# Performance work log

Measured on AMD Instinct MI355X. Metric: run time of the kernel, lower is better.

## Reference

```python
import jax, jax.numpy as jnp
import numpy as np

B, T, DIM, H, DH = 4, 4096, 1024, 16, 64


def setup_inputs() -> dict:
    key = jax.random.key(0)
    ks = jax.random.split(key, 6)
    s = lambda fan_in: 1.0 / np.sqrt(fan_in)
    x = jax.random.normal(ks[0], (B, T, DIM), dtype=jnp.float32)
    Wq = jax.random.uniform(ks[1], (DIM, H * DH), jnp.float32, -s(DIM), s(DIM))
    Wk = jax.random.uniform(ks[2], (DIM, H * DH), jnp.float32, -s(DIM), s(DIM))
    Wv = jax.random.uniform(ks[3], (DIM, H * DH), jnp.float32, -s(DIM), s(DIM))
    Wo = jax.random.uniform(ks[4], (H * DH, DIM), jnp.float32, -s(H * DH), s(H * DH))
    bo = jax.random.uniform(ks[5], (DIM,), jnp.float32, -s(H * DH), s(H * DH))
    return {"x": x, "Wq": Wq, "Wk": Wk, "Wv": Wv, "Wo": Wo, "bo": bo}


def reference(x, Wq, Wk, Wv, Wo, bo):
    b, t, _ = x.shape
    # projections (no bias, matching nn.Linear(bias=False))
    to_heads = lambda y: y.reshape(b, t, H, DH).transpose(0, 2, 1, 3)  # bhnd
    q = to_heads(x @ Wq)
    k = to_heads(x @ Wk)
    v = to_heads(x @ Wv)
    # linear attention: softmax over feature dim for q, over seq dim for k
    q = jax.nn.softmax(q, axis=-1) * (DH ** -0.5)
    k = jax.nn.softmax(k, axis=-2)
    context = jnp.einsum('bhnd,bhne->bhde', k, v)   # [b,h,dh,dh]
    attn = jnp.einsum('bhnd,bhde->bhne', q, context)  # [b,h,n,dh]
    attn = attn.transpose(0, 2, 1, 3).reshape(b, t, H * DH)
    return attn @ Wo + bo  # dropout is identity at p=0.0 / eval
```

## Files before the change

kernel.cpp:

```cpp
#include <hip/hip_runtime.h>
#include <hip/hip_bf16.h>
#include <cstdint>
#include <cstddef>

#define BB 4
#define TT 4096
#define HH 16
#define NROWS 16384

typedef __attribute__((ext_vector_type(8))) short bf16x8;
typedef __attribute__((ext_vector_type(4))) float f32x4;

__device__ __forceinline__ void gload_lds16(const void* g, void* l) {
  __builtin_amdgcn_global_load_lds(
      (const __attribute__((address_space(1))) void*)g,
      (__attribute__((address_space(3))) void*)l, 16, 0, 0);
}

template <int N>
__device__ __forceinline__ void wait_vmcnt() {
  if constexpr (N == 4)
    asm volatile("s_waitcnt vmcnt(4)" ::: "memory");
  else
    asm volatile("s_waitcnt vmcnt(0)" ::: "memory");
  __builtin_amdgcn_sched_barrier(0);
}

__device__ __forceinline__ void hbar() {
  asm volatile("s_barrier" ::: "memory");
  __builtin_amdgcn_sched_barrier(0);
}

__global__ __launch_bounds__(256) void xconv_k(const float* __restrict__ x,
                                               __hip_bfloat16* __restrict__ xb) {
  const size_t i = ((size_t)blockIdx.x * 256 + threadIdx.x) * 8;
  float4 a = *(const float4*)&x[i];
  float4 b = *(const float4*)&x[i + 4];
  __hip_bfloat16 o[8] __attribute__((aligned(16)));
  o[0] = __float2bfloat16(a.x); o[1] = __float2bfloat16(a.y);
  o[2] = __float2bfloat16(a.z); o[3] = __float2bfloat16(a.w);
  o[4] = __float2bfloat16(b.x); o[5] = __float2bfloat16(b.y);
  o[6] = __float2bfloat16(b.z); o[7] = __float2bfloat16(b.w);
  *(int4*)&xb[i] = *(const int4*)o;
}

__global__ __launch_bounds__(256) void wconv_k(const float* __restrict__ Wq,
                                               const float* __restrict__ Wk,
                                               const float* __restrict__ Wv,
                                               const float* __restrict__ Wo,
                                               __hip_bfloat16* __restrict__ WT) {
  const int which = blockIdx.z;
  const float* W = which == 0 ? Wq : which == 1 ? Wk : which == 2 ? Wv : Wo;
  __shared__ float tile[64][65];
  const int n0 = blockIdx.x * 64, k0 = blockIdx.y * 64;
  const int t = threadIdx.x;
  const int r = t >> 2;
  const int cq = (t & 3) * 16;
#pragma unroll
  for (int i = 0; i < 4; ++i) {
    float4 v = *(const float4*)&W[(size_t)(k0 + r) * 1024 + n0 + cq + i * 4];
    tile[r][cq + i * 4 + 0] = v.x;
    tile[r][cq + i * 4 + 1] = v.y;
    tile[r][cq + i * 4 + 2] = v.z;
    tile[r][cq + i * 4 + 3] = v.w;
  }
  __syncthreads();
  __hip_bfloat16 ob[16] __attribute__((aligned(16)));
#pragma unroll
  for (int j = 0; j < 16; ++j) ob[j] = __float2bfloat16(tile[cq + j][r]);
  __hip_bfloat16* dst = WT + (size_t)(which * 1024 + n0 + r) * 1024 + k0 + cq;
  *(int4*)dst = *(const int4*)&ob[0];
  *(int4*)(dst + 8) = *(const int4*)&ob[8];
}

template <int OMODE, int PB>
__global__ __launch_bounds__(512) void mgemm3_k(
    const __hip_bfloat16* __restrict__ A, int lda,
    const __hip_bfloat16* __restrict__ BT, const float* __restrict__ bias,
    void* __restrict__ Cp, int ldc, int gx) {
  __shared__ __hip_bfloat16 lds[2][32768];

  const int t = threadIdx.x;
  const int wid = t >> 6, l = t & 63;
  const int wr = wid >> 2, wc = wid & 3;

  const int nwg = gridDim.x;
  const int cpx = nwg >> 3;
  const int bid = blockIdx.x;
  const int swz = (bid & 7) * cpx + (bid >> 3);
  const int bx = swz % gx, by = swz / gx;
  const int row0 = by * 256, col0 = bx * 256;

  const __hip_bfloat16* BTb = PB ? BT + ((size_t)(row0 >> 12) << 20) : BT;

  const int sg = l >> 3;
  const int octp = ((l & 7) + sg) & 7;
  const int koct = octp & 3;
  const int srow = 2 * (wid * 16 + sg) + (octp >> 2);
  const __hip_bfloat16* As0 = A + (size_t)(row0 + srow) * lda + koct * 8;
  const __hip_bfloat16* Bs0 = BTb + (size_t)(col0 + srow) * 1024 + koct * 8;

  f32x4 acc[8][4];
#pragma unroll
  for (int m = 0; m < 8; ++m)
#pragma unroll
    for (int n = 0; n < 4; ++n) acc[m][n] = (f32x4){0.f, 0.f, 0.f, 0.f};

  const int lr = l & 15, hk = l >> 4;
  const int slot = (((lr & 1) << 2) + hk - (lr >> 1)) & 7;
  const int rdo = (lr >> 1) * 64 + slot * 8;

  auto stageA = [&](int tn, int c) {
    __hip_bfloat16* d = &lds[tn & 1][c * 8192 + wid * 1024];
    const __hip_bfloat16* s = As0 + tn * 64 + c * 32;
    gload_lds16(s, d);
    gload_lds16(s + (size_t)16 * lda, d + 512);
  };
  auto stageB = [&](int tn, int c) {
    __hip_bfloat16* d = &lds[tn & 1][16384 + c * 8192 + wid * 1024];
    const __hip_bfloat16* s = Bs0 + tn * 64 + c * 32;
    gload_lds16(s, d);
    gload_lds16(s + (size_t)16 * 1024, d + 512);
  };

  stageA(0, 0); stageB(0, 0); stageA(0, 1); stageB(0, 1);

  const __hip_bfloat16* sb = &lds[0][0];
  for (int tn = 0; tn < 16; ++tn) {
    const int bufo = (tn & 1) * 32768;
    const bool pre = tn < 15;
    bf16x8 bfv[4], afv[4];

    wait_vmcnt<4>();
    hbar();
    if (pre) stageA(tn + 1, 0);
#pragma unroll
    for (int n = 0; n < 4; ++n)
      bfv[n] = *(const bf16x8*)(sb + bufo + 16384 + wc * 2048 + n * 512 + rdo);
#pragma unroll
    for (int j = 0; j < 4; ++j)
      afv[j] = *(const bf16x8*)(sb + bufo + wr * 4096 + j * 512 + rdo);
    __builtin_amdgcn_s_setprio(1);
#pragma unroll
    for (int j = 0; j < 4; ++j)
#pragma unroll
      for (int n = 0; n < 4; ++n)
        acc[j][n] = __builtin_amdgcn_mfma_f32_16x16x32_bf16(afv[j], bfv[n],
                                                            acc[j][n], 0, 0, 0);
    __builtin_amdgcn_s_setprio(0);
    if (pre) stageB(tn + 1, 0);
#pragma unroll
    for (int j = 0; j < 4; ++j)
      afv[j] = *(const bf16x8*)(sb + bufo + wr * 4096 + 2048 + j * 512 + rdo);
    __builtin_amdgcn_s_setprio(1);
#pragma unroll
    for (int j = 0; j < 4; ++j)
#pragma unroll
      for (int n = 0; n < 4; ++n)
        acc[4 + j][n] = __builtin_amdgcn_mfma_f32_16x16x32_bf16(
            afv[j], bfv[n], acc[4 + j][n], 0, 0, 0);
    __builtin_amdgcn_s_setprio(0);

    if (pre)
      wait_vmcnt<4>();
    else
      wait_vmcnt<0>();
    hbar();
    if (pre) stageA(tn + 1, 1);
#pragma unroll
    for (int n = 0; n < 4; ++n)
      bfv[n] = *(const bf16x8*)(sb + bufo + 8192 + 16384 + wc * 2048 +
                                n * 512 + rdo);
#pragma unroll
    for (int j = 0; j < 4; ++j)
      afv[j] = *(const bf16x8*)(sb + bufo + 8192 + wr * 4096 + j * 512 + rdo);
    __builtin_amdgcn_s_setprio(1);
#pragma unroll
    for (int j = 0; j < 4; ++j)
#pragma unroll
      for (int n = 0; n < 4; ++n)
        acc[j][n] = __builtin_amdgcn_mfma_f32_16x16x32_bf16(afv[j], bfv[n],
                                                            acc[j][n], 0, 0, 0);
    __builtin_amdgcn_s_setprio(0);
    if (pre) stageB(tn + 1, 1);
#pragma unroll
    for (int j = 0; j < 4; ++j)
      afv[j] = *(const bf16x8*)(sb + bufo + 8192 + wr * 4096 + 2048 + j * 512 +
                                rdo);
    __builtin_amdgcn_s_setprio(1);
#pragma unroll
    for (int j = 0; j < 4; ++j)
#pragma unroll
      for (int n = 0; n < 4; ++n)
        acc[4 + j][n] = __builtin_amdgcn_mfma_f32_16x16x32_bf16(
            afv[j], bfv[n], acc[4 + j][n], 0, 0, 0);
    __builtin_amdgcn_s_setprio(0);
  }

  const int cr = hk * 4;
  const int cc = lr;
  if constexpr (OMODE == 0) {
    __hip_bfloat16* C = (__hip_bfloat16*)Cp;
#pragma unroll
    for (int m = 0; m < 8; ++m)
#pragma unroll
      for (int n = 0; n < 4; ++n) {
        const size_t cb = (size_t)(row0 + wr * 128 + m * 16 + cr) * ldc +
                          col0 + wc * 64 + n * 16 + cc;
#pragma unroll
        for (int j = 0; j < 4; ++j)
          C[cb + (size_t)j * ldc] = __float2bfloat16(acc[m][n][j]);
      }
  } else {
    float* C = (float*)Cp;
    float bv[4];
#pragma unroll
    for (int n = 0; n < 4; ++n) bv[n] = bias[col0 + wc * 64 + n * 16 + cc];
#pragma unroll
    for (int m = 0; m < 8; ++m)
#pragma unroll
      for (int n = 0; n < 4; ++n) {
        const size_t cb = (size_t)(row0 + wr * 128 + m * 16 + cr) * ldc +
                          col0 + wc * 64 + n * 16 + cc;
#pragma unroll
        for (int j = 0; j < 4; ++j)
          C[cb + (size_t)j * ldc] = acc[m][n][j] + bv[n];
      }
  }
}

__global__ __launch_bounds__(256) void ctxq_k(__hip_bfloat16* __restrict__ qkv,
                                              float* __restrict__ part,
                                              float* __restrict__ den) {
  __shared__ __hip_bfloat16 ldsb[2 * 8736];
  __hip_bfloat16* ekT = ldsb;
  __hip_bfloat16* vfT = ldsb + 8736;

  const int bh = blockIdx.x;
  const int s = blockIdx.y;
  const int b = bh >> 4;
  const int h = bh & 15;
  const int n0 = s * 128;
  const int t = threadIdx.x;

  const int rr = t >> 1;
  const int c0 = (t & 1) * 32;
  const size_t base = (size_t)(b * TT + n0 + rr) * 3072 + 1024 + h * 64 + c0;
  int4 kq[4], vq[4];
#pragma unroll
  for (int i = 0; i < 4; ++i) {
    kq[i] = *(const int4*)(qkv + base + i * 8);
    vq[i] = *(const int4*)(qkv + base + 1024 + i * 8);
  }

  {
    const int g8 = t >> 3;
    const int lc = (t & 7) * 8;
#pragma unroll
    for (int it = 0; it < 4; ++it) {
      const int r = it * 32 + g8;
      __hip_bfloat16* p =
          qkv + (size_t)(b * TT + n0 + r) * 3072 + h * 64 + lc;
      int4 raw = *(const int4*)p;
      const __hip_bfloat16* bp = (const __hip_bfloat16*)&raw;
      float v[8];
      float m = -1e30f;
#pragma unroll
      for (int j = 0; j < 8; ++j) {
        v[j] = __bfloat162float(bp[j]);
        m = fmaxf(m, v[j]);
      }
      m = fmaxf(m, __shfl_xor(m, 1));
      m = fmaxf(m, __shfl_xor(m, 2));
      m = fmaxf(m, __shfl_xor(m, 4));
      float sm = 0.f;
#pragma unroll
      for (int j = 0; j < 8; ++j) {
        v[j] = __expf(v[j] - m);
        sm += v[j];
      }
      sm += __shfl_xor(sm, 1);
      sm += __shfl_xor(sm, 2);
      sm += __shfl_xor(sm, 4);
      const float inv = 0.125f / sm;
      __hip_bfloat16 o[8] __attribute__((aligned(16)));
#pragma unroll
      for (int j = 0; j < 8; ++j) o[j] = __float2bfloat16(v[j] * inv);
      *(int4*)p = *(const int4*)o;
    }
  }

#pragma unroll
  for (int i = 0; i < 4; ++i) {
    const __hip_bfloat16* kp = (const __hip_bfloat16*)&kq[i];
    const __hip_bfloat16* vp = (const __hip_bfloat16*)&vq[i];
#pragma unroll
    for (int j = 0; j < 8; ++j) {
      const int c = c0 + i * 8 + j;
      const int off = c * 136 + ((c >> 5) & 1) * 32 + rr;
      ekT[off] = __float2bfloat16(__expf(__bfloat162float(kp[j])));
      vfT[off] = vp[j];
    }
  }
  __syncthreads();

  const int w = t >> 6, l = t & 63;
  const int lr = l & 15, hk = l >> 4;
  f32x4 acc[4];
#pragma unroll
  for (int n = 0; n < 4; ++n) acc[n] = (f32x4){0.f, 0.f, 0.f, 0.f};

  const int arow = w * 16 + lr;
  const int abase = arow * 136 + ((arow >> 5) & 1) * 32 + hk * 8;
#pragma unroll
  for (int ks = 0; ks < 4; ++ks) {
    bf16x8 af = *(const bf16x8*)(ekT + abase + ks * 32);
#pragma unroll
    for (int n = 0; n < 4; ++n) {
      const int brow = n * 16 + lr;
      bf16x8 bf = *(const bf16x8*)(vfT + brow * 136 + ((brow >> 5) & 1) * 32 +
                                   hk * 8 + ks * 32);
      acc[n] =
          __builtin_amdgcn_mfma_f32_16x16x32_bf16(af, bf, acc[n], 0, 0, 0);
    }
  }

  float* pb = part + ((size_t)bh * 32 + s) * 4096;
#pragma unroll
  for (int n = 0; n < 4; ++n)
#pragma unroll
    for (int j = 0; j < 4; ++j)
      pb[(w * 16 + hk * 4 + j) * 64 + n * 16 + lr] = acc[n][j];

  if ((t & 3) == 0) {
    const int d = t >> 2;
    const int dbase = d * 136 + ((d >> 5) & 1) * 32;
    float sden = 0.f;
#pragma unroll
    for (int q8 = 0; q8 < 16; ++q8) {
      bf16x8 e8 = *(const bf16x8*)(ekT + dbase + q8 * 8);
      const __hip_bfloat16* ep = (const __hip_bfloat16*)&e8;
#pragma unroll
      for (int j = 0; j < 8; ++j) sden += __bfloat162float(ep[j]);
    }
    den[((size_t)bh * 32 + s) * 64 + d] = sden;
  }
}

__global__ __launch_bounds__(256) void ctx_reduce_k(
    const float* __restrict__ part, const float* __restrict__ den,
    __hip_bfloat16* __restrict__ ctxb) {
  const int bh = blockIdx.x, q = blockIdx.y, t = threadIdx.x;
  const int idx = q * 1024 + t * 4;
  const int d = idx >> 6;
  float sden = 0.f;
  for (int s = 0; s < 32; ++s) sden += den[((size_t)bh * 32 + s) * 64 + d];
  float4 sv = {0.f, 0.f, 0.f, 0.f};
  const float* pb = part + (size_t)bh * 32 * 4096 + idx;
  for (int s = 0; s < 32; ++s) {
    float4 v = *(const float4*)(pb + (size_t)s * 4096);
    sv.x += v.x; sv.y += v.y; sv.z += v.z; sv.w += v.w;
  }
  const float di = 1.0f / sden;
  __hip_bfloat16 ob[4] __attribute__((aligned(8)));
  ob[0] = __float2bfloat16(sv.x * di);
  ob[1] = __float2bfloat16(sv.y * di);
  ob[2] = __float2bfloat16(sv.z * di);
  ob[3] = __float2bfloat16(sv.w * di);
  *(int2*)&ctxb[(size_t)bh * 4096 + idx] = *(const int2*)ob;
}

__global__ __launch_bounds__(256) void wfuse_k(
    const __hip_bfloat16* __restrict__ WT,
    const __hip_bfloat16* __restrict__ ctxb, __hip_bfloat16* __restrict__ WfT) {
  const int bh = blockIdx.x;
  const int b = bh >> 4, h = bh & 15;
  const int t = threadIdx.x, w = t >> 6, l = t & 63;
  const int n1 = blockIdx.y * 64 + w * 16;
  const int lr = l & 15, hk = l >> 4;

  f32x4 acc[4];
#pragma unroll
  for (int n = 0; n < 4; ++n) acc[n] = (f32x4){0.f, 0.f, 0.f, 0.f};

  const __hip_bfloat16* Abase =
      WT + (size_t)(3072 + n1 + lr) * 1024 + h * 64 + hk * 8;
  const __hip_bfloat16* Bbase = ctxb + (size_t)bh * 4096 + hk * 8;

#pragma unroll
  for (int kk2 = 0; kk2 < 2; ++kk2) {
    bf16x8 af = *(const bf16x8*)(Abase + kk2 * 32);
#pragma unroll
    for (int n = 0; n < 4; ++n) {
      bf16x8 bf = *(const bf16x8*)(Bbase + (n * 16 + lr) * 64 + kk2 * 32);
      acc[n] = __builtin_amdgcn_mfma_f32_16x16x32_bf16(af, bf, acc[n], 0, 0, 0);
    }
  }

  __hip_bfloat16* W0 = WfT + ((size_t)b << 20) + (size_t)(n1 + hk * 4) * 1024 +
                       h * 64 + lr;
#pragma unroll
  for (int n = 0; n < 4; ++n)
#pragma unroll
    for (int j = 0; j < 4; ++j)
      W0[(size_t)j * 1024 + n * 16] = __float2bfloat16(acc[n][j]);
}

extern "C" void kernel_launch(void* const* d_in, const int* in_sizes, int n_in,
                              void* d_out, int out_size, void* d_ws,
                              size_t ws_size, hipStream_t stream) {
  const float* x = (const float*)d_in[0];
  const float* Wq = (const float*)d_in[1];
  const float* Wk = (const float*)d_in[2];
  const float* Wv = (const float*)d_in[3];
  const float* Wo = (const float*)d_in[4];
  const float* bo = (const float*)d_in[5];
  float* out = (float*)d_out;

  char* ws = (char*)d_ws;
  __hip_bfloat16* qkv = (__hip_bfloat16*)ws;
  __hip_bfloat16* WT = (__hip_bfloat16*)(ws + 100663296ull);
  float* den = (float*)(ws + 100663296ull + 8388608ull);
  __hip_bfloat16* ctxb =
      (__hip_bfloat16*)(ws + 100663296ull + 8388608ull + 524288ull);
  __hip_bfloat16* WfT =
      (__hip_bfloat16*)(ws + 100663296ull + 8388608ull + 1048576ull);
  __hip_bfloat16* xb = (__hip_bfloat16*)d_out;
  float* part = (float*)((char*)d_out + 33554432ull);

  const dim3 blk(256);

  xconv_k<<<dim3(NROWS * 1024 / 8 / 256), blk, 0, stream>>>(x, xb);
  wconv_k<<<dim3(16, 16, 4), blk, 0, stream>>>(Wq, Wk, Wv, Wo, WT);

  mgemm3_k<0, 0><<<dim3(768), dim3(512), 0, stream>>>(xb, 1024, WT, nullptr,
                                                      qkv, 3072, 12);

  ctxq_k<<<dim3(64, 32), blk, 0, stream>>>(qkv, part, den);
  ctx_reduce_k<<<dim3(64, 4), blk, 0, stream>>>(part, den, ctxb);
  wfuse_k<<<dim3(64, 16), blk, 0, stream>>>(WT, ctxb, WfT);

  mgemm3_k<1, 1><<<dim3(256), dim3(512), 0, stream>>>(qkv, 3072, WfT, bo, out,
                                                      1024, 4);
}
```

Baseline: 195.4 us.

## Use 4-stage LDS pipeline in GEMM and fuse Q softmax into QKV epilogue

The GEMM drops its 2-buffer, 64-wide K-step scheme for a 4-slot ring of 32-wide K-steps, keeping three stages of global-to-LDS loads in flight and needing one barrier per step. The QKV GEMM epilogue now applies the per-head feature softmax and scaling to Q in registers, using cross-lane shuffles, before storing. This removes the separate read-modify-write pass over Q in the context kernel, which now only reads qkv. The costs are more barriers per unit of K, extra exp and shuffle work in the Q-column tiles, and Q being rounded to bf16 after the softmax instead of before it.

Result: slower. 203.3 us (+4.0%).

```diff
diff --git a/kernel.cpp b/kernel.cpp
--- a/kernel.cpp
+++ b/kernel.cpp
@@ -19,7 +19,9 @@
 
 template <int N>
 __device__ __forceinline__ void wait_vmcnt() {
-  if constexpr (N == 4)
+  if constexpr (N == 8)
+    asm volatile("s_waitcnt vmcnt(8)" ::: "memory");
+  else if constexpr (N == 4)
     asm volatile("s_waitcnt vmcnt(4)" ::: "memory");
   else
     asm volatile("s_waitcnt vmcnt(0)" ::: "memory");
@@ -73,12 +75,12 @@
   *(int4*)(dst + 8) = *(const int4*)&ob[8];
 }
 
-template <int OMODE, int PB>
-__global__ __launch_bounds__(512) void mgemm3_k(
+template <int OMODE, int PB, int QSM>
+__global__ __launch_bounds__(512) void mgemm4_k(
     const __hip_bfloat16* __restrict__ A, int lda,
     const __hip_bfloat16* __restrict__ BT, const float* __restrict__ bias,
     void* __restrict__ Cp, int ldc, int gx) {
-  __shared__ __hip_bfloat16 lds[2][32768];
+  __shared__ __hip_bfloat16 lds[4][16384];
 
   const int t = threadIdx.x;
   const int wid = t >> 6, l = t & 63;
@@ -110,36 +112,25 @@
   const int slot = (((lr & 1) << 2) + hk - (lr >> 1)) & 7;
   const int rdo = (lr >> 1) * 64 + slot * 8;
 
-  auto stageA = [&](int tn, int c) {
-    __hip_bfloat16* d = &lds[tn & 1][c * 8192 + wid * 1024];
-    const __hip_bfloat16* s = As0 + tn * 64 + c * 32;
-    gload_lds16(s, d);
-    gload_lds16(s + (size_t)16 * lda, d + 512);
+  auto stage = [&](int u) {
+    __hip_bfloat16* d = &lds[u & 3][wid * 1024];
+    const __hip_bfloat16* sa = As0 + u * 32;
+    const __hip_bfloat16* sb = Bs0 + u * 32;
+    gload_lds16(sa, d);
+    gload_lds16(sa + (size_t)16 * lda, d + 512);
+    gload_lds16(sb, d + 8192);
+    gload_lds16(sb + (size_t)16 * 1024, d + 8192 + 512);
   };
-  auto stageB = [&](int tn, int c) {
-    __hip_bfloat16* d = &lds[tn & 1][16384 + c * 8192 + wid * 1024];
-    const __hip_bfloat16* s = Bs0 + tn * 64 + c * 32;
-    gload_lds16(s, d);
-    gload_lds16(s + (size_t)16 * 1024, d + 512);
-  };
-
-  stageA(0, 0); stageB(0, 0); stageA(0, 1); stageB(0, 1);
-
-  const __hip_bfloat16* sb = &lds[0][0];
-  for (int tn = 0; tn < 16; ++tn) {
-    const int bufo = (tn & 1) * 32768;
-    const bool pre = tn < 15;
+
+  auto compute = [&](int sl) {
+    const __hip_bfloat16* s = &lds[sl][0];
     bf16x8 bfv[4], afv[4];
-
-    wait_vmcnt<4>();
-    hbar();
-    if (pre) stageA(tn + 1, 0);
 #pragma unroll
     for (int n = 0; n < 4; ++n)
-      bfv[n] = *(const bf16x8*)(sb + bufo + 16384 + wc * 2048 + n * 512 + rdo);
-#pragma unroll
-    for (int j = 0; j < 4; ++j)
-      afv[j] = *(const bf16x8*)(sb + bufo + wr * 4096 + j * 512 + rdo);
+      bfv[n] = *(const bf16x8*)(s + 8192 + wc * 2048 + n * 512 + rdo);
+#pragma unroll
+    for (int j = 0; j < 4; ++j)
+      afv[j] = *(const bf16x8*)(s + wr * 4096 + j * 512 + rdo);
     __builtin_amdgcn_s_setprio(1);
 #pragma unroll
     for (int j = 0; j < 4; ++j)
@@ -148,10 +139,9 @@
         acc[j][n] = __builtin_amdgcn_mfma_f32_16x16x32_bf16(afv[j], bfv[n],
                                                             acc[j][n], 0, 0, 0);
     __builtin_amdgcn_s_setprio(0);
-    if (pre) stageB(tn + 1, 0);
-#pragma unroll
-    for (int j = 0; j < 4; ++j)
-      afv[j] = *(const bf16x8*)(sb + bufo + wr * 4096 + 2048 + j * 512 + rdo);
+#pragma unroll
+    for (int j = 0; j < 4; ++j)
+      afv[j] = *(const bf16x8*)(s + wr * 4096 + 2048 + j * 512 + rdo);
     __builtin_amdgcn_s_setprio(1);
 #pragma unroll
     for (int j = 0; j < 4; ++j)
@@ -160,46 +150,53 @@
         acc[4 + j][n] = __builtin_amdgcn_mfma_f32_16x16x32_bf16(
             afv[j], bfv[n], acc[4 + j][n], 0, 0, 0);
     __builtin_amdgcn_s_setprio(0);
-
-    if (pre)
-      wait_vmcnt<4>();
-    else
-      wait_vmcnt<0>();
+  };
+
+  stage(0); stage(1); stage(2);
+
+#pragma unroll 4
+  for (int u = 0; u < 28; ++u) {
+    wait_vmcnt<8>();
     hbar();
-    if (pre) stageA(tn + 1, 1);
-#pragma unroll
-    for (int n = 0; n < 4; ++n)
-      bfv[n] = *(const bf16x8*)(sb + bufo + 8192 + 16384 + wc * 2048 +
-                                n * 512 + rdo);
-#pragma unroll
-    for (int j = 0; j < 4; ++j)
-      afv[j] = *(const bf16x8*)(sb + bufo + 8192 + wr * 4096 + j * 512 + rdo);
-    __builtin_amdgcn_s_setprio(1);
-#pragma unroll
-    for (int j = 0; j < 4; ++j)
-#pragma unroll
-      for (int n = 0; n < 4; ++n)
-        acc[j][n] = __builtin_amdgcn_mfma_f32_16x16x32_bf16(afv[j], bfv[n],
-                                                            acc[j][n], 0, 0, 0);
-    __builtin_amdgcn_s_setprio(0);
-    if (pre) stageB(tn + 1, 1);
-#pragma unroll
-    for (int j = 0; j < 4; ++j)
-      afv[j] = *(const bf16x8*)(sb + bufo + 8192 + wr * 4096 + 2048 + j * 512 +
-                                rdo);
-    __builtin_amdgcn_s_setprio(1);
-#pragma unroll
-    for (int j = 0; j < 4; ++j)
-#pragma unroll
-      for (int n = 0; n < 4; ++n)
-        acc[4 + j][n] = __builtin_amdgcn_mfma_f32_16x16x32_bf16(
-            afv[j], bfv[n], acc[4 + j][n], 0, 0, 0);
-    __builtin_amdgcn_s_setprio(0);
-  }
+    stage(u + 3);
+    compute(u & 3);
+  }
+  wait_vmcnt<8>(); hbar(); stage(31); compute(0);
+  wait_vmcnt<8>(); hbar(); compute(1);
+  wait_vmcnt<4>(); hbar(); compute(2);
+  wait_vmcnt<0>(); hbar(); compute(3);
 
   const int cr = hk * 4;
   const int cc = lr;
   if constexpr (OMODE == 0) {
+    if (QSM && col0 < 1024) {
+#pragma unroll
+      for (int m = 0; m < 8; ++m) {
+#pragma unroll
+        for (int j = 0; j < 4; ++j) {
+          float mx = fmaxf(fmaxf(acc[m][0][j], acc[m][1][j]),
+                           fmaxf(acc[m][2][j], acc[m][3][j]));
+          mx = fmaxf(mx, __shfl_xor(mx, 1));
+          mx = fmaxf(mx, __shfl_xor(mx, 2));
+          mx = fmaxf(mx, __shfl_xor(mx, 4));
+          mx = fmaxf(mx, __shfl_xor(mx, 8));
+          float e0 = __expf(acc[m][0][j] - mx);
+          float e1 = __expf(acc[m][1][j] - mx);
+          float e2 = __expf(acc[m][2][j] - mx);
+          float e3 = __expf(acc[m][3][j] - mx);
+          float sm = e0 + e1 + e2 + e3;
+          sm += __shfl_xor(sm, 1);
+          sm += __shfl_xor(sm, 2);
+          sm += __shfl_xor(sm, 4);
+          sm += __shfl_xor(sm, 8);
+          const float inv = 0.125f / sm;
+          acc[m][0][j] = e0 * inv;
+          acc[m][1][j] = e1 * inv;
+          acc[m][2][j] = e2 * inv;
+          acc[m][3][j] = e3 * inv;
+        }
+      }
+    }
     __hip_bfloat16* C = (__hip_bfloat16*)Cp;
 #pragma unroll
     for (int m = 0; m < 8; ++m)
@@ -229,9 +226,9 @@
   }
 }
 
-__global__ __launch_bounds__(256) void ctxq_k(__hip_bfloat16* __restrict__ qkv,
-                                              float* __restrict__ part,
-                                              float* __restrict__ den) {
+__global__ __launch_bounds__(256) void ctxkv_k(
+    const __hip_bfloat16* __restrict__ qkv, float* __restrict__ part,
+    float* __restrict__ den) {
   __shared__ __hip_bfloat16 ldsb[2 * 8736];
   __hip_bfloat16* ekT = ldsb;
   __hip_bfloat16* vfT = ldsb + 8736;
@@ -251,43 +248,6 @@
   for (int i = 0; i < 4; ++i) {
     kq[i] = *(const int4*)(qkv + base + i * 8);
     vq[i] = *(const int4*)(qkv + base + 1024 + i * 8);
-  }
-
-  {
-    const int g8 = t >> 3;
-    const int lc = (t & 7) * 8;
-#pragma unroll
-    for (int it = 0; it < 4; ++it) {
-      const int r = it * 32 + g8;
-      __hip_bfloat16* p =
-          qkv + (size_t)(b * TT + n0 + r) * 3072 + h * 64 + lc;
-      int4 raw = *(const int4*)p;
-      const __hip_bfloat16* bp = (const __hip_bfloat16*)&raw;
-      float v[8];
-      float m = -1e30f;
-#pragma unroll
-      for (int j = 0; j < 8; ++j) {
-        v[j] = __bfloat162float(bp[j]);
-        m = fmaxf(m, v[j]);
-      }
-      m = fmaxf(m, __shfl_xor(m, 1));
-      m = fmaxf(m, __shfl_xor(m, 2));
-      m = fmaxf(m, __shfl_xor(m, 4));
-      float sm = 0.f;
-#pragma unroll
-      for (int j = 0; j < 8; ++j) {
-        v[j] = __expf(v[j] - m);
-        sm += v[j];
-      }
-      sm += __shfl_xor(sm, 1);
-      sm += __shfl_xor(sm, 2);
-      sm += __shfl_xor(sm, 4);
-      const float inv = 0.125f / sm;
-      __hip_bfloat16 o[8] __attribute__((aligned(16)));
-#pragma unroll
-      for (int j = 0; j < 8; ++j) o[j] = __float2bfloat16(v[j] * inv);
-      *(int4*)p = *(const int4*)o;
-    }
   }
 
 #pragma unroll
@@ -433,13 +393,13 @@
   xconv_k<<<dim3(NROWS * 1024 / 8 / 256), blk, 0, stream>>>(x, xb);
   wconv_k<<<dim3(16, 16, 4), blk, 0, stream>>>(Wq, Wk, Wv, Wo, WT);
 
-  mgemm3_k<0, 0><<<dim3(768), dim3(512), 0, stream>>>(xb, 1024, WT, nullptr,
-                                                      qkv, 3072, 12);
-
-  ctxq_k<<<dim3(64, 32), blk, 0, stream>>>(qkv, part, den);
+  mgemm4_k<0, 0, 1><<<dim3(768), dim3(512), 0, stream>>>(xb, 1024, WT, nullptr,
+                                                         qkv, 3072, 12);
+
+  ctxkv_k<<<dim3(64, 32), blk, 0, stream>>>(qkv, part, den);
   ctx_reduce_k<<<dim3(64, 4), blk, 0, stream>>>(part, den, ctxb);
   wfuse_k<<<dim3(64, 16), blk, 0, stream>>>(WT, ctxb, WfT);
 
-  mgemm3_k<1, 1><<<dim3(256), dim3(512), 0, stream>>>(qkv, 3072, WfT, bo, out,
-                                                      1024, 4);
-}
+  mgemm4_k<1, 1, 0><<<dim3(256), dim3(512), 0, stream>>>(qkv, 3072, WfT, bo,
+                                                         out, 1024, 4);
+}
```
